# Kernel optimization log

Hardware: AMD Instinct MI355X
Metric: run time of the kernel (lower is better)

Reference implementation:

```python
import jax, jax.numpy as jnp
import numpy as np

N_NODES = 100000
N_EDGES = 1000000
D = 64
N_GRAPHS = 512


def setup_inputs() -> dict:
    key = jax.random.key(0)
    k1, k2, k3, k4, k5 = jax.random.split(key, 5)
    x = jax.random.normal(k1, (N_NODES, D), dtype=jnp.float32)
    edge_index = jax.random.randint(k2, (2, N_EDGES), 0, N_NODES, dtype=jnp.int64)
    edge_attr = jax.random.uniform(k3, (N_EDGES,), dtype=jnp.float32)
    batch = jnp.sort(jax.random.randint(k4, (N_NODES,), 0, N_GRAPHS, dtype=jnp.int64))
    W = jax.random.normal(k5, (1, D), dtype=jnp.float32) / np.sqrt(D)
    b = jnp.zeros((1,), dtype=jnp.float32)
    return {"x": x, "edge_index": edge_index, "edge_attr": edge_attr, "batch": batch, "W": W, "b": b}


def reference(x, edge_index, edge_attr, batch, W, b):
    src, dst = edge_index[0], edge_index[1]
    # SimpleConv (aggr='sum'): out[v] = sum_{(u,v) in E} edge_attr_e * x[u]
    msgs = x[src] * edge_attr[:, None]                      # [E, D]
    agg = jax.ops.segment_sum(msgs, dst, num_segments=N_NODES)  # [N, D]
    # global_mean_pool over batch ids
    sums = jax.ops.segment_sum(agg, batch, num_segments=N_GRAPHS)  # [G, D]
    counts = jax.ops.segment_sum(jnp.ones((N_NODES,), dtype=x.dtype), batch, num_segments=N_GRAPHS)
    pooled = sums / jnp.maximum(counts, 1.0)[:, None]       # [G, D]
    # Linear(hidden_channels, 1)
    return pooled @ W.T + b                                 # [G, 1]
```

## Files before the change

kernel.cpp:

```cpp
#include <hip/hip_runtime.h>

#define N_NODES 100000
#define N_EDGES 1000000
#define D 64
#define N_GRAPHS 512
#define DOT_THREADS (N_NODES * 16)
#define DOT_BLOCKS (DOT_THREADS / 256)
#define TAIL_BLOCKS 4
#define K2_THREADS 1024
#define K2_BLOCKS ((N_EDGES / 4 + K2_THREADS - 1) / K2_THREADS)

__global__ __launch_bounds__(256) void dot_kernel(const float* __restrict__ x,
                                                  const float* __restrict__ W,
                                                  const int* __restrict__ batch,
                                                  const float* __restrict__ bptr,
                                                  float* __restrict__ y,
                                                  float* __restrict__ inv_cnt,
                                                  float* __restrict__ out) {
    __shared__ int slb[132];
    if (blockIdx.x < DOT_BLOCKS) {
        int t = blockIdx.x * 256 + threadIdx.x;
        int v = t >> 4;
        int sub = t & 15;
        const float4 xv = *reinterpret_cast<const float4*>(x + (size_t)v * D + sub * 4);
        const float4 wv = *reinterpret_cast<const float4*>(W + sub * 4);
        float p = xv.x * wv.x + xv.y * wv.y + xv.z * wv.z + xv.w * wv.w;
        p += __shfl_xor(p, 1, 64);
        p += __shfl_xor(p, 2, 64);
        p += __shfl_xor(p, 4, 64);
        p += __shfl_xor(p, 8, 64);
        if (sub == 0) y[v] = p;
        return;
    }
    const int tb = blockIdx.x - DOT_BLOCKS;
    const int gbase = tb * 128;
    const int t = threadIdx.x;
    if (t <= 128) {
        const int target = gbase + t;
        int lo = 0, hi = N_NODES;
        while (lo < hi) {
            int mid = (lo + hi) >> 1;
            if (batch[mid] < target) lo = mid + 1; else hi = mid;
        }
        slb[t] = lo;
    }
    __syncthreads();
    if (t < 128) {
        const int g = gbase + t;
        float cnt = (float)(slb[t + 1] - slb[t]);
        inv_cnt[g] = 1.0f / fmaxf(cnt, 1.0f);
        out[g] = bptr[0];
    }
}

__global__ __launch_bounds__(K2_THREADS) void edge_kernel(const int* __restrict__ ei,
                                                          const float* __restrict__ ea,
                                                          const int* __restrict__ batch,
                                                          const float* __restrict__ y,
                                                          const float* __restrict__ inv_cnt,
                                                          float* __restrict__ out) {
    __shared__ float sacc[N_GRAPHS];
    const int tid = threadIdx.x;
    if (tid < N_GRAPHS) sacc[tid] = 0.0f;
    __syncthreads();

    int idx = blockIdx.x * K2_THREADS + tid;
    if (idx < N_EDGES / 4) {
        const int4   s4 = reinterpret_cast<const int4*>(ei)[idx];
        const int4   d4 = reinterpret_cast<const int4*>(ei + N_EDGES)[idx];
        const float4 a4 = reinterpret_cast<const float4*>(ea)[idx];
        float m0 = a4.x * y[s4.x];  int g0 = batch[d4.x];
        float m1 = a4.y * y[s4.y];  int g1 = batch[d4.y];
        float m2 = a4.z * y[s4.z];  int g2 = batch[d4.z];
        float m3 = a4.w * y[s4.w];  int g3 = batch[d4.w];
        atomicAdd(&sacc[g0], m0);
        atomicAdd(&sacc[g1], m1);
        atomicAdd(&sacc[g2], m2);
        atomicAdd(&sacc[g3], m3);
    }
    __syncthreads();
    if (tid < N_GRAPHS) {
        float v = sacc[tid];
        if (v != 0.0f) atomicAdd(&out[tid], v * inv_cnt[tid]);
    }
}

extern "C" void kernel_launch(void* const* d_in, const int* in_sizes, int n_in,
                              void* d_out, int out_size, void* d_ws, size_t ws_size,
                              hipStream_t stream) {
    const float* x     = (const float*)d_in[0];
    const int*   ei    = (const int*)  d_in[1];
    const float* ea    = (const float*)d_in[2];
    const int*   batch = (const int*)  d_in[3];
    const float* W     = (const float*)d_in[4];
    const float* b     = (const float*)d_in[5];
    float* out = (float*)d_out;

    float* y       = (float*)d_ws;
    float* inv_cnt = y + N_NODES;

    dot_kernel<<<DOT_BLOCKS + TAIL_BLOCKS, 256, 0, stream>>>(
        x, W, batch, b, y, inv_cnt, out);
    edge_kernel<<<K2_BLOCKS, K2_THREADS, 0, stream>>>(ei, ea, batch, y, inv_cnt, out);
}
```

Before: 102.4 us.

## Fuse dot and edge kernels into one cooperative kernel with grid sync

```diff
diff --git a/kernel.cpp b/kernel.cpp
--- a/kernel.cpp
+++ b/kernel.cpp
@@ -1,14 +1,85 @@
 #include <hip/hip_runtime.h>
+#include <hip/hip_cooperative_groups.h>
 
 #define N_NODES 100000
 #define N_EDGES 1000000
 #define D 64
 #define N_GRAPHS 512
-#define DOT_THREADS (N_NODES * 16)
-#define DOT_BLOCKS (DOT_THREADS / 256)
+#define NVEC (N_EDGES / 4)
+#define DOT_ITEMS (N_NODES * 16)
+#define BLK 1024
+#define GRID 256
+#define NTHREADS (BLK * GRID)
+
+namespace cg = cooperative_groups;
+
+__global__ __launch_bounds__(BLK, 4) void fused_kernel(
+    const float* __restrict__ x, const float* __restrict__ W,
+    const int* __restrict__ ei, const float* __restrict__ ea,
+    const int* __restrict__ batch, const float* __restrict__ bptr,
+    float* __restrict__ y, int* __restrict__ lb,
+    float* __restrict__ out) {
+    __shared__ float sacc[N_GRAPHS];
+    const int tid = threadIdx.x;
+    const int gt  = blockIdx.x * BLK + tid;
+
+    if (tid < N_GRAPHS) sacc[tid] = 0.0f;
+    if (blockIdx.x == 0 && tid < N_GRAPHS) out[tid] = bptr[0];
+
+    int4 s4, d4; float4 a4;
+    const bool has_edge = gt < NVEC;
+    if (has_edge) {
+        s4 = reinterpret_cast<const int4*>(ei)[gt];
+        d4 = reinterpret_cast<const int4*>(ei + N_EDGES)[gt];
+        a4 = reinterpret_cast<const float4*>(ea)[gt];
+    }
+
+    int sg = -1;
+    if (tid < 2) sg = blockIdx.x * 2 + tid;
+    else if (tid == 2 && blockIdx.x == 0) sg = N_GRAPHS;
+    if (sg >= 0) {
+        int lo = 0, hi = N_NODES;
+        while (lo < hi) { int mid = (lo + hi) >> 1; if (batch[mid] < sg) lo = mid + 1; else hi = mid; }
+        lb[sg] = lo;
+    }
+
+    const int sub = tid & 15;
+    const float4 wv = *reinterpret_cast<const float4*>(W + sub * 4);
+    for (int t = gt; t < DOT_ITEMS; t += NTHREADS) {
+        const int v = t >> 4;
+        const float4 xv = *reinterpret_cast<const float4*>(x + (size_t)v * D + sub * 4);
+        float p = xv.x * wv.x + xv.y * wv.y + xv.z * wv.z + xv.w * wv.w;
+        p += __shfl_xor(p, 1, 64);
+        p += __shfl_xor(p, 2, 64);
+        p += __shfl_xor(p, 4, 64);
+        p += __shfl_xor(p, 8, 64);
+        if (sub == 0) y[v] = p;
+    }
+
+    cg::this_grid().sync();
+
+    if (has_edge) {
+        float m0 = a4.x * y[s4.x];  int g0 = batch[d4.x];
+        float m1 = a4.y * y[s4.y];  int g1 = batch[d4.y];
+        float m2 = a4.z * y[s4.z];  int g2 = batch[d4.z];
+        float m3 = a4.w * y[s4.w];  int g3 = batch[d4.w];
+        atomicAdd(&sacc[g0], m0);
+        atomicAdd(&sacc[g1], m1);
+        atomicAdd(&sacc[g2], m2);
+        atomicAdd(&sacc[g3], m3);
+    }
+    __syncthreads();
+    if (tid < N_GRAPHS) {
+        float v = sacc[tid];
+        float cnt = (float)(lb[tid + 1] - lb[tid]);
+        if (v != 0.0f) atomicAdd(&out[tid], v * (1.0f / fmaxf(cnt, 1.0f)));
+    }
+}
+
+#define DOT_BLOCKS (DOT_ITEMS / 256)
 #define TAIL_BLOCKS 4
 #define K2_THREADS 1024
-#define K2_BLOCKS ((N_EDGES / 4 + K2_THREADS - 1) / K2_THREADS)
+#define K2_BLOCKS ((NVEC + K2_THREADS - 1) / K2_THREADS)
 
 __global__ __launch_bounds__(256) void dot_kernel(const float* __restrict__ x,
                                                   const float* __restrict__ W,
@@ -38,10 +109,7 @@
     if (t <= 128) {
         const int target = gbase + t;
         int lo = 0, hi = N_NODES;
-        while (lo < hi) {
-            int mid = (lo + hi) >> 1;
-            if (batch[mid] < target) lo = mid + 1; else hi = mid;
-        }
+        while (lo < hi) { int mid = (lo + hi) >> 1; if (batch[mid] < target) lo = mid + 1; else hi = mid; }
         slb[t] = lo;
     }
     __syncthreads();
@@ -63,9 +131,8 @@
     const int tid = threadIdx.x;
     if (tid < N_GRAPHS) sacc[tid] = 0.0f;
     __syncthreads();
-
     int idx = blockIdx.x * K2_THREADS + tid;
-    if (idx < N_EDGES / 4) {
+    if (idx < NVEC) {
         const int4   s4 = reinterpret_cast<const int4*>(ei)[idx];
         const int4   d4 = reinterpret_cast<const int4*>(ei + N_EDGES)[idx];
         const float4 a4 = reinterpret_cast<const float4*>(ea)[idx];
@@ -97,9 +164,16 @@
     float* out = (float*)d_out;
 
     float* y       = (float*)d_ws;
-    float* inv_cnt = y + N_NODES;
+    int*   lb      = (int*)(y + N_NODES);
+    float* inv_cnt = (float*)(lb + N_GRAPHS + 4);
 
-    dot_kernel<<<DOT_BLOCKS + TAIL_BLOCKS, 256, 0, stream>>>(
-        x, W, batch, b, y, inv_cnt, out);
-    edge_kernel<<<K2_BLOCKS, K2_THREADS, 0, stream>>>(ei, ea, batch, y, inv_cnt, out);
+    void* args[] = {(void*)&x, (void*)&W, (void*)&ei, (void*)&ea,
+                    (void*)&batch, (void*)&b, (void*)&y, (void*)&lb, (void*)&out};
+    hipError_t err = hipLaunchCooperativeKernel((const void*)fused_kernel,
+                                                dim3(GRID), dim3(BLK), args, 0, stream);
+    if (err != hipSuccess) {
+        dot_kernel<<<DOT_BLOCKS + TAIL_BLOCKS, 256, 0, stream>>>(
+            x, W, batch, b, y, inv_cnt, out);
+        edge_kernel<<<K2_BLOCKS, K2_THREADS, 0, stream>>>(ei, ea, batch, y, inv_cnt, out);
+    }
 }
```

Result: slower. 146.4 us (+42.9%).
